# Kernel tuning notes

Hardware: AMD Instinct MI355X
Metric: run time of the kernel (lower is better)

The kernel has to match this reference:

```python
import jax, jax.numpy as jnp
import numpy as np
from math import sqrt

INPUT_SIZE = 1024
HIDDEN_SIZE = 1024
OUTPUT_SIZE = 512
BATCH = 64
SEQ = 512


def _uniform(key, shape, stdv):
    return jax.random.uniform(key, shape, jnp.float32, -stdv, stdv)


def setup_inputs() -> dict:
    key = jax.random.key(0)
    ks = jax.random.split(key, 20)
    stdv = 1.0 / sqrt(HIDDEN_SIZE)
    H, I, O = HIDDEN_SIZE, INPUT_SIZE, OUTPUT_SIZE
    inp = {
        "X": jax.random.normal(ks[0], (BATCH, SEQ, I), jnp.float32),
        "c0": jnp.zeros((H, 1), jnp.float32),
        "h0": jnp.zeros((H, 1), jnp.float32),
        "w_hi": _uniform(ks[1], (H, H), stdv), "w_xi": _uniform(ks[2], (H, I), stdv),
        "b_hi": _uniform(ks[3], (H, 1), stdv), "b_xi": _uniform(ks[4], (H, 1), stdv),
        "w_hf": _uniform(ks[5], (H, H), stdv), "w_xf": _uniform(ks[6], (H, I), stdv),
        "b_hf": _uniform(ks[7], (H, 1), stdv), "b_xf": _uniform(ks[8], (H, 1), stdv),
        "w_ho": _uniform(ks[9], (H, H), stdv), "w_xo": _uniform(ks[10], (H, I), stdv),
        "b_ho": _uniform(ks[11], (H, 1), stdv), "b_xo": _uniform(ks[12], (H, 1), stdv),
        "w_hg": _uniform(ks[13], (H, H), stdv), "w_xg": _uniform(ks[14], (H, I), stdv),
        "b_hg": _uniform(ks[15], (H, 1), stdv), "b_xg": _uniform(ks[16], (H, 1), stdv),
        "w": _uniform(ks[17], (O, H), stdv),
    }
    return inp


def reference(X, c0, h0,
              w_hi, w_xi, b_hi, b_xi,
              w_hf, w_xf, b_hf, b_xf,
              w_ho, w_xo, b_ho, b_xo,
              w_hg, w_xg, b_hg, b_xg, w):
    B = X.shape[0]
    # state kept as (B, H); biases squeezed to (H,)
    bi = (b_hi + b_xi)[:, 0]
    bf = (b_hf + b_xf)[:, 0]
    bo = (b_ho + b_xo)[:, 0]
    bg = (b_hg + b_xg)[:, 0]
    h0b = jnp.broadcast_to(h0[:, 0], (B, h0.shape[0]))
    c0b = jnp.broadcast_to(c0[:, 0], (B, c0.shape[0]))

    def step(carry, x_t):  # x_t: (B, I)
        h, c = carry
        i = jax.nn.sigmoid(h @ w_hi.T + x_t @ w_xi.T + bi)
        f = jax.nn.sigmoid(h @ w_hf.T + x_t @ w_xf.T + bf)
        o = jax.nn.sigmoid(h @ w_ho.T + x_t @ w_xo.T + bo)
        g = jnp.tanh(h @ w_hg.T + x_t @ w_xg.T + bg)
        c = f * c + i * g
        h = o * jnp.tanh(c)
        return (h, c), None

    (h, c), _ = jax.lax.scan(step, (h0b, c0b), jnp.swapaxes(X, 0, 1))
    out = h @ w.T  # (B, O)
    return out[:, :, None]  # match torch output shape (B, O, 1)
```

## Files before the change

kernel.cpp:

```cpp
#include <hip/hip_runtime.h>


typedef short short8 __attribute__((ext_vector_type(8)));
typedef float f32x4 __attribute__((ext_vector_type(4)));

typedef __attribute__((address_space(1))) const unsigned int glb_u32;
typedef __attribute__((address_space(3))) unsigned int lds_u32;

#define SEQL  512
#define POISON 0xFFFFFFFFFFFFFFFFull
#define BUFU64 16384

__device__ __forceinline__ unsigned short f2bf(float f) {
    unsigned int u = __builtin_bit_cast(unsigned int, f);
    u += 0x7FFFu + ((u >> 16) & 1u);
    return (unsigned short)(u >> 16);
}
__device__ __forceinline__ float bf2f(unsigned short s) {
    unsigned int u = ((unsigned int)s) << 16;
    return __builtin_bit_cast(float, u);
}
__device__ __forceinline__ float sigmoidf_fast(float x) {
    return 1.f / (1.f + __expf(-x));
}
__device__ __forceinline__ float tanhf_fast(float x) {
    return 1.f - 2.f / (1.f + __expf(2.f * x));
}
__device__ __forceinline__ void gld_lds16(const unsigned short* g, unsigned short* l) {
    __builtin_amdgcn_global_load_lds((glb_u32*)g, (lds_u32*)l, 16, 0, 0);
}

__global__ void k_pack_w(const float* __restrict__ w0, const float* __restrict__ w1,
                         const float* __restrict__ w2, const float* __restrict__ w3,
                         unsigned short* __restrict__ dst) {
    int idx4 = blockIdx.x * blockDim.x + threadIdx.x;
    int np = idx4 >> 8;
    int k4 = (idx4 & 255) * 4;
    int g = np & 3, r = np >> 2;
    const float* src = (g == 0) ? w0 : (g == 1) ? w1 : (g == 2) ? w2 : w3;
    float4 v = *(const float4*)(src + r * 1024 + k4);
    ushort4 o;
    o.x = f2bf(v.x); o.y = f2bf(v.y); o.z = f2bf(v.z); o.w = f2bf(v.w);
    *(ushort4*)(dst + (size_t)np * 1024 + k4) = o;
}

__global__ void k_misc(const float* __restrict__ b_hi, const float* __restrict__ b_xi,
                       const float* __restrict__ b_hf, const float* __restrict__ b_xf,
                       const float* __restrict__ b_ho, const float* __restrict__ b_xo,
                       const float* __restrict__ b_hg, const float* __restrict__ b_xg,
                       const float* __restrict__ h0, const float* __restrict__ w,
                       float* __restrict__ bias, unsigned short* __restrict__ hbuf,
                       float* __restrict__ wT) {
    int idx = blockIdx.x * blockDim.x + threadIdx.x;
    if (idx < 4096) {
        int g = idx & 3, r = idx >> 2;
        const float* bh = (g == 0) ? b_hi : (g == 1) ? b_hf : (g == 2) ? b_ho : b_hg;
        const float* bx = (g == 0) ? b_xi : (g == 1) ? b_xf : (g == 2) ? b_xo : b_xg;
        bias[idx] = bh[r] + bx[r];
    } else if (idx < 4096 + 65536) {
        int e = idx - 4096;
        int cg = e >> 8;
        int h16 = e & 15;
        hbuf[e] = f2bf(h0[(cg & 63) * 16 + h16]);
    } else if (idx < 4096 + 65536 + 524288) {
        int e = idx - 69632;
        int k = e >> 9, o = e & 511;
        wT[e] = w[o * 1024 + k];
    } else if (idx < 4096 + 65536 + 524288 + 3 * BUFU64) {
        int e = idx - (4096 + 65536 + 524288);
        ((unsigned long long*)hbuf)[BUFU64 + e] = POISON;
    }
}

__global__ void k_convert_x(const float* __restrict__ X, unsigned short* __restrict__ Xb) {
    int idx = blockIdx.x * blockDim.x + threadIdx.x;
    float4 v = ((const float4*)X)[idx];
    ushort4 o;
    o.x = f2bf(v.x); o.y = f2bf(v.y); o.z = f2bf(v.z); o.w = f2bf(v.w);
    ((ushort4*)Xb)[idx] = o;
}

__global__ __launch_bounds__(256, 1) void k_rec(const unsigned short* __restrict__ Wh,
                                                const unsigned short* __restrict__ Wx,
                                                const unsigned short* __restrict__ Xb,
                                                const float* __restrict__ bias,
                                                const float* __restrict__ c0,
                                                unsigned short* __restrict__ hbuf) {
    const int blk = blockIdx.x;
    const int jb  = blk & 3;
    const int ibb = blk >> 2;
    const int tid = threadIdx.x;
    const int w   = tid >> 6;
    const int l   = tid & 63;
    const int l15 = l & 15, lq = l >> 4;

    __shared__ unsigned short hTl[16 * 1032];
    __shared__ unsigned short xTl[16 * 1032];
    __shared__ unsigned short hTr[16 * 20];

    short8 afragH[32], afragX[32];
    {
        const unsigned short* wrH = Wh + (size_t)(ibb * 64 + w * 16 + l15) * 1024;
        const unsigned short* wrX = Wx + (size_t)(ibb * 64 + w * 16 + l15) * 1024;
#pragma unroll
        for (int ks = 0; ks < 32; ++ks)
            afragH[ks] = *(const short8*)(wrH + ks * 32 + lq * 8);
#pragma unroll
        for (int ks = 0; ks < 32; ++ks)
            afragX[ks] = *(const short8*)(wrX + ks * 32 + lq * 8);
#pragma unroll
        for (int ks = 0; ks < 32; ++ks)
            asm volatile("" : "+v"(afragH[ks]));
    }

    const int hid = ibb * 16 + w * 4 + lq;
    float c = c0[hid];
    float bias4[4];
#pragma unroll
    for (int rr = 0; rr < 4; ++rr)
        bias4[rr] = bias[(size_t)ibb * 64 + w * 16 + lq * 4 + rr];

    unsigned long long* hb64 = (unsigned long long*)hbuf;

    const int sbb = (tid >> 2) & 15, sl4 = tid & 3;
    const int stage_sh = sbb * 1032 + w * 16 + sl4 * 4;

#pragma unroll
    for (int i = 0; i < 8; ++i) {
        int r = w * 8 + i, b16 = r >> 1, half = r & 1;
        const unsigned short* src =
            Xb + ((size_t)(jb * 16 + b16) * 512 + 0) * 1024 + half * 512 + l * 8;
        gld_lds16(src, &xTl[b16 * 1032 + half * 512]);
    }
    asm volatile("s_waitcnt vmcnt(0)" ::: "memory");
    __syncthreads();

    float xg[4];
    {
        f32x4 xa0 = {0.f, 0.f, 0.f, 0.f}, xa1 = {0.f, 0.f, 0.f, 0.f};
#pragma unroll
        for (int ks = 0; ks < 32; ks += 2) {
            short8 b0 = *(const short8*)(&xTl[l15 * 1032 + ks * 32 + lq * 8]);
            short8 b1 = *(const short8*)(&xTl[l15 * 1032 + (ks + 1) * 32 + lq * 8]);
            xa0 = __builtin_amdgcn_mfma_f32_16x16x32_bf16(afragX[ks], b0, xa0, 0, 0, 0);
            xa1 = __builtin_amdgcn_mfma_f32_16x16x32_bf16(afragX[ks + 1], b1, xa1, 0, 0, 0);
        }
#pragma unroll
        for (int rr = 0; rr < 4; ++rr)
            xg[rr] = xa0[rr] + xa1[rr] + bias4[rr];
    }

    for (int t = 0; t < SEQL; ++t) {
        {
            const unsigned long long* src =
                hb64 + (size_t)(t & 3) * BUFU64 + (size_t)jb * 4096 + tid;
            unsigned long long tmp[16];
#pragma unroll
            for (int p = 0; p < 16; ++p)
                tmp[p] = __hip_atomic_load(src + p * 256, __ATOMIC_RELAXED,
                                           __HIP_MEMORY_SCOPE_AGENT);
            for (;;) {
                unsigned miss = 0;
#pragma unroll
                for (int p = 0; p < 16; ++p)
                    if (tmp[p] == POISON) miss |= 1u << p;
                if (!miss) break;
                __builtin_amdgcn_s_sleep(1);
#pragma unroll
                for (int p = 0; p < 16; ++p)
                    if (miss & (1u << p))
                        tmp[p] = __hip_atomic_load(src + p * 256, __ATOMIC_RELAXED,
                                                   __HIP_MEMORY_SCOPE_AGENT);
            }
#pragma unroll
            for (int p = 0; p < 16; ++p)
                *(unsigned long long*)(&hTl[stage_sh + p * 64]) = tmp[p];
        }
        __syncthreads();

        if (t < SEQL - 1) {
#pragma unroll
            for (int i = 0; i < 8; ++i) {
                int r = w * 8 + i, b16 = r >> 1, half = r & 1;
                const unsigned short* src =
                    Xb + ((size_t)(jb * 16 + b16) * 512 + (t + 1)) * 1024 + half * 512 + l * 8;
                gld_lds16(src, &xTl[b16 * 1032 + half * 512]);
            }
        }

        {
            f32x4 a0 = {0.f, 0.f, 0.f, 0.f}, a1 = {0.f, 0.f, 0.f, 0.f};
#pragma unroll
            for (int ks = 0; ks < 32; ks += 2) {
                short8 b0 = *(const short8*)(&hTl[l15 * 1032 + ks * 32 + lq * 8]);
                short8 b1 = *(const short8*)(&hTl[l15 * 1032 + (ks + 1) * 32 + lq * 8]);
                a0 = __builtin_amdgcn_mfma_f32_16x16x32_bf16(afragH[ks], b0, a0, 0, 0, 0);
                a1 = __builtin_amdgcn_mfma_f32_16x16x32_bf16(afragH[ks + 1], b1, a1, 0, 0, 0);
            }
            float pi = a0[0] + a1[0] + xg[0];
            float pf = a0[1] + a1[1] + xg[1];
            float po = a0[2] + a1[2] + xg[2];
            float pg = a0[3] + a1[3] + xg[3];
            float ig = sigmoidf_fast(pi);
            float fg = sigmoidf_fast(pf);
            float og = sigmoidf_fast(po);
            float gg = tanhf_fast(pg);
            c = fg * c + ig * gg;
            float hh = og * tanhf_fast(c);
            hTr[l15 * 20 + w * 4 + lq] = f2bf(hh);
        }
        __syncthreads();

        if (tid < 64) {
            int b = tid >> 2, l4 = tid & 3;
            unsigned long long v = *(const unsigned long long*)(&hTr[b * 20 + l4 * 4]);
            asm volatile("s_waitcnt vmcnt(0)" ::: "memory");
            size_t u = (size_t)(jb * 64 + ibb) * 64 + b * 4 + l4;
            __hip_atomic_store(hb64 + (size_t)((t + 1) & 3) * BUFU64 + u, v,
                               __ATOMIC_RELAXED, __HIP_MEMORY_SCOPE_AGENT);
            __hip_atomic_store(hb64 + (size_t)((t + 3) & 3) * BUFU64 + u, POISON,
                               __ATOMIC_RELAXED, __HIP_MEMORY_SCOPE_AGENT);
        }

        if (t < SEQL - 1) {
            f32x4 xa0 = {0.f, 0.f, 0.f, 0.f}, xa1 = {0.f, 0.f, 0.f, 0.f};
#pragma unroll
            for (int ks = 0; ks < 32; ks += 2) {
                short8 b0 = *(const short8*)(&xTl[l15 * 1032 + ks * 32 + lq * 8]);
                short8 b1 = *(const short8*)(&xTl[l15 * 1032 + (ks + 1) * 32 + lq * 8]);
                xa0 = __builtin_amdgcn_mfma_f32_16x16x32_bf16(afragX[ks], b0, xa0, 0, 0, 0);
                xa1 = __builtin_amdgcn_mfma_f32_16x16x32_bf16(afragX[ks + 1], b1, xa1, 0, 0, 0);
            }
#pragma unroll
            for (int rr = 0; rr < 4; ++rr)
                xg[rr] = xa0[rr] + xa1[rr] + bias4[rr];
        }
    }
}

__global__ __launch_bounds__(256) void k_out(const unsigned short* __restrict__ hT,
                                             const float* __restrict__ wT,
                                             float* __restrict__ out) {
    const int b = blockIdx.x;
    const int jb = b >> 4, b16 = b & 15;
    const int tid = threadIdx.x;
    __shared__ float hs[1024];
#pragma unroll
    for (int p = 0; p < 4; ++p) {
        int k = p * 256 + tid;
        hs[k] = bf2f(hT[(size_t)(jb * 64 + (k >> 4)) * 256 + b16 * 16 + (k & 15)]);
    }
    __syncthreads();
    float a0 = 0.f, a1 = 0.f;
    for (int k = 0; k < 1024; ++k) {
        float hv = hs[k];
        a0 = fmaf(hv, wT[k * 512 + tid], a0);
        a1 = fmaf(hv, wT[k * 512 + 256 + tid], a1);
    }
    out[b * 512 + tid] = a0;
    out[b * 512 + 256 + tid] = a1;
}

extern "C" void kernel_launch(void* const* d_in, const int* in_sizes, int n_in,
                              void* d_out, int out_size, void* d_ws, size_t ws_size,
                              hipStream_t stream) {
    const float* X    = (const float*)d_in[0];
    const float* c0   = (const float*)d_in[1];
    const float* h0   = (const float*)d_in[2];
    const float* w_hi = (const float*)d_in[3];
    const float* w_xi = (const float*)d_in[4];
    const float* b_hi = (const float*)d_in[5];
    const float* b_xi = (const float*)d_in[6];
    const float* w_hf = (const float*)d_in[7];
    const float* w_xf = (const float*)d_in[8];
    const float* b_hf = (const float*)d_in[9];
    const float* b_xf = (const float*)d_in[10];
    const float* w_ho = (const float*)d_in[11];
    const float* w_xo = (const float*)d_in[12];
    const float* b_ho = (const float*)d_in[13];
    const float* b_xo = (const float*)d_in[14];
    const float* w_hg = (const float*)d_in[15];
    const float* w_xg = (const float*)d_in[16];
    const float* b_hg = (const float*)d_in[17];
    const float* b_xg = (const float*)d_in[18];
    const float* w    = (const float*)d_in[19];

    char* ws = (char*)d_ws;
    size_t off = 0;
    unsigned short* Whp = (unsigned short*)(ws + off); off += (size_t)4096 * 1024 * 2;
    unsigned short* Wxp = (unsigned short*)(ws + off); off += (size_t)4096 * 1024 * 2;
    unsigned short* Xb  = (unsigned short*)(ws + off); off += (size_t)64 * 512 * 1024 * 2;
    float*          bias= (float*)(ws + off);          off += (size_t)4096 * 4;
    float*          wT  = (float*)(ws + off);          off += (size_t)1024 * 512 * 4;
    unsigned short* hbuf= (unsigned short*)(ws + off); off += (size_t)4 * 64 * 1024 * 2;
    if (ws_size < off) return;

    k_pack_w<<<4096, 256, 0, stream>>>(w_hi, w_hf, w_ho, w_hg, Whp);
    k_pack_w<<<4096, 256, 0, stream>>>(w_xi, w_xf, w_xo, w_xg, Wxp);
    k_misc<<<(4096 + 65536 + 524288 + 3 * BUFU64 + 255) / 256, 256, 0, stream>>>(
        b_hi, b_xi, b_hf, b_xf, b_ho, b_xo, b_hg, b_xg, h0, w, bias, hbuf, wT);
    k_convert_x<<<33554432 / 4 / 256, 256, 0, stream>>>(X, Xb);

    k_rec<<<dim3(256), dim3(256), 0, stream>>>(Whp, Wxp, Xb, bias, c0, hbuf);

    k_out<<<64, 256, 0, stream>>>(hbuf, wT, (float*)d_out);
}
```

Measured before the change: 1.820 ms.

## Split recurrent kernel into hidden and input warp groups with pipelined x-projection

Doubles the block size of the recurrent kernel so four warps hold the recurrent weight fragments and four separate warps hold the input weight fragments. The input-projection warps prefetch X two steps ahead and compute the next step's x-gates into a double-buffered LDS array while the hidden warps poll for h and run the recurrent MFMA plus gate math. This takes the x-projection off the serial critical path and halves per-thread register pressure from weight fragments. In exchange, block-wide syncs now include twice as many waves, and the pipeline adds warm-up iterations.

```diff
diff --git a/kernel.cpp b/kernel.cpp
--- a/kernel.cpp
+++ b/kernel.cpp
@@ -80,7 +80,7 @@
     ((ushort4*)Xb)[idx] = o;
 }
 
-__global__ __launch_bounds__(256, 1) void k_rec(const unsigned short* __restrict__ Wh,
+__global__ __launch_bounds__(512, 1) void k_rec(const unsigned short* __restrict__ Wh,
                                                 const unsigned short* __restrict__ Wx,
                                                 const unsigned short* __restrict__ Xb,
                                                 const float* __restrict__ bias,
@@ -91,123 +91,144 @@
     const int ibb = blk >> 2;
     const int tid = threadIdx.x;
     const int w   = tid >> 6;
+    const int wq  = w & 3;
+    const bool hw = (w < 4);
     const int l   = tid & 63;
     const int l15 = l & 15, lq = l >> 4;
 
     __shared__ unsigned short hTl[16 * 1032];
     __shared__ unsigned short xTl[16 * 1032];
+    __shared__ f32x4 xgbuf[2][256];
     __shared__ unsigned short hTr[16 * 20];
 
-    short8 afragH[32], afragX[32];
+    short8 afrag[32];
     {
-        const unsigned short* wrH = Wh + (size_t)(ibb * 64 + w * 16 + l15) * 1024;
-        const unsigned short* wrX = Wx + (size_t)(ibb * 64 + w * 16 + l15) * 1024;
+        const unsigned short* wsrc = hw ? Wh : Wx;
+        const unsigned short* wrow = wsrc + (size_t)(ibb * 64 + wq * 16 + l15) * 1024;
 #pragma unroll
         for (int ks = 0; ks < 32; ++ks)
-            afragH[ks] = *(const short8*)(wrH + ks * 32 + lq * 8);
+            afrag[ks] = *(const short8*)(wrow + ks * 32 + lq * 8);
 #pragma unroll
         for (int ks = 0; ks < 32; ++ks)
-            afragX[ks] = *(const short8*)(wrX + ks * 32 + lq * 8);
-#pragma unroll
-        for (int ks = 0; ks < 32; ++ks)
-            asm volatile("" : "+v"(afragH[ks]));
-    }
-
-    const int hid = ibb * 16 + w * 4 + lq;
+            asm volatile("" : "+v"(afrag[ks]));
+    }
+
+    const int hid = ibb * 16 + wq * 4 + lq;
     float c = c0[hid];
     float bias4[4];
 #pragma unroll
     for (int rr = 0; rr < 4; ++rr)
-        bias4[rr] = bias[(size_t)ibb * 64 + w * 16 + lq * 4 + rr];
+        bias4[rr] = bias[(size_t)ibb * 64 + wq * 16 + lq * 4 + rr];
 
     unsigned long long* hb64 = (unsigned long long*)hbuf;
 
-    const int sbb = (tid >> 2) & 15, sl4 = tid & 3;
-    const int stage_sh = sbb * 1032 + w * 16 + sl4 * 4;
-
-#pragma unroll
-    for (int i = 0; i < 8; ++i) {
-        int r = w * 8 + i, b16 = r >> 1, half = r & 1;
-        const unsigned short* src =
-            Xb + ((size_t)(jb * 16 + b16) * 512 + 0) * 1024 + half * 512 + l * 8;
-        gld_lds16(src, &xTl[b16 * 1032 + half * 512]);
-    }
-    asm volatile("s_waitcnt vmcnt(0)" ::: "memory");
-    __syncthreads();
-
-    float xg[4];
-    {
-        f32x4 xa0 = {0.f, 0.f, 0.f, 0.f}, xa1 = {0.f, 0.f, 0.f, 0.f};
-#pragma unroll
-        for (int ks = 0; ks < 32; ks += 2) {
-            short8 b0 = *(const short8*)(&xTl[l15 * 1032 + ks * 32 + lq * 8]);
-            short8 b1 = *(const short8*)(&xTl[l15 * 1032 + (ks + 1) * 32 + lq * 8]);
-            xa0 = __builtin_amdgcn_mfma_f32_16x16x32_bf16(afragX[ks], b0, xa0, 0, 0, 0);
-            xa1 = __builtin_amdgcn_mfma_f32_16x16x32_bf16(afragX[ks + 1], b1, xa1, 0, 0, 0);
-        }
-#pragma unroll
-        for (int rr = 0; rr < 4; ++rr)
-            xg[rr] = xa0[rr] + xa1[rr] + bias4[rr];
-    }
-
-    for (int t = 0; t < SEQL; ++t) {
-        {
-            const unsigned long long* src =
-                hb64 + (size_t)(t & 3) * BUFU64 + (size_t)jb * 4096 + tid;
-            unsigned long long tmp[16];
-#pragma unroll
-            for (int p = 0; p < 16; ++p)
-                tmp[p] = __hip_atomic_load(src + p * 256, __ATOMIC_RELAXED,
-                                           __HIP_MEMORY_SCOPE_AGENT);
-            for (;;) {
-                unsigned miss = 0;
+    const int stage_sh = ((tid >> 2) & 15) * 1032 + wq * 16 + (tid & 3) * 4;
+
+    for (int t = -3; t < SEQL; ++t) {
+        if (t >= 0) {
+            if (hw) {
+                const unsigned long long* src =
+                    hb64 + (size_t)(t & 3) * BUFU64 + (size_t)jb * 4096 + tid;
+                unsigned long long tmp[16];
 #pragma unroll
                 for (int p = 0; p < 16; ++p)
-                    if (tmp[p] == POISON) miss |= 1u << p;
-                if (!miss) break;
-                __builtin_amdgcn_s_sleep(1);
+                    tmp[p] = __hip_atomic_load(src + p * 256, __ATOMIC_RELAXED,
+                                               __HIP_MEMORY_SCOPE_AGENT);
+                for (;;) {
+                    unsigned miss = 0;
+#pragma unroll
+                    for (int p = 0; p < 16; ++p)
+                        if (tmp[p] == POISON) miss |= 1u << p;
+                    if (!miss) break;
+                    __builtin_amdgcn_s_sleep(1);
+#pragma unroll
+                    for (int p = 0; p < 16; ++p)
+                        if (miss & (1u << p))
+                            tmp[p] = __hip_atomic_load(src + p * 256, __ATOMIC_RELAXED,
+                                                       __HIP_MEMORY_SCOPE_AGENT);
+                }
 #pragma unroll
                 for (int p = 0; p < 16; ++p)
-                    if (miss & (1u << p))
-                        tmp[p] = __hip_atomic_load(src + p * 256, __ATOMIC_RELAXED,
-                                                   __HIP_MEMORY_SCOPE_AGENT);
-            }
-#pragma unroll
-            for (int p = 0; p < 16; ++p)
-                *(unsigned long long*)(&hTl[stage_sh + p * 64]) = tmp[p];
+                    *(unsigned long long*)(&hTl[stage_sh + p * 64]) = tmp[p];
+            } else if (t < SEQL - 1) {
+                f32x4 xa0 = {0.f, 0.f, 0.f, 0.f}, xa1 = {0.f, 0.f, 0.f, 0.f};
+#pragma unroll
+                for (int ks = 0; ks < 32; ks += 2) {
+                    short8 b0 = *(const short8*)(&xTl[l15 * 1032 + ks * 32 + lq * 8]);
+                    short8 b1 = *(const short8*)(&xTl[l15 * 1032 + (ks + 1) * 32 + lq * 8]);
+                    xa0 = __builtin_amdgcn_mfma_f32_16x16x32_bf16(afrag[ks], b0, xa0, 0, 0, 0);
+                    xa1 = __builtin_amdgcn_mfma_f32_16x16x32_bf16(afrag[ks + 1], b1, xa1, 0, 0, 0);
+                }
+                f32x4 xg4;
+#pragma unroll
+                for (int rr = 0; rr < 4; ++rr)
+                    xg4[rr] = xa0[rr] + xa1[rr] + bias4[rr];
+                xgbuf[(t + 1) & 1][wq * 64 + l] = xg4;
+            }
+        } else if (t == -3 || t == -1) {
+            if (!hw) {
+                const int tt = (t == -3) ? 0 : 1;
+#pragma unroll
+                for (int i = 0; i < 8; ++i) {
+                    int r = wq * 8 + i, b16 = r >> 1, half = r & 1;
+                    const unsigned short* src =
+                        Xb + ((size_t)(jb * 16 + b16) * 512 + tt) * 1024 + half * 512 + l * 8;
+                    gld_lds16(src, &xTl[b16 * 1032 + half * 512]);
+                }
+                asm volatile("s_waitcnt vmcnt(0)" ::: "memory");
+            }
+        } else {
+            if (!hw) {
+                f32x4 xa0 = {0.f, 0.f, 0.f, 0.f}, xa1 = {0.f, 0.f, 0.f, 0.f};
+#pragma unroll
+                for (int ks = 0; ks < 32; ks += 2) {
+                    short8 b0 = *(const short8*)(&xTl[l15 * 1032 + ks * 32 + lq * 8]);
+                    short8 b1 = *(const short8*)(&xTl[l15 * 1032 + (ks + 1) * 32 + lq * 8]);
+                    xa0 = __builtin_amdgcn_mfma_f32_16x16x32_bf16(afrag[ks], b0, xa0, 0, 0, 0);
+                    xa1 = __builtin_amdgcn_mfma_f32_16x16x32_bf16(afrag[ks + 1], b1, xa1, 0, 0, 0);
+                }
+                f32x4 xg4;
+#pragma unroll
+                for (int rr = 0; rr < 4; ++rr)
+                    xg4[rr] = xa0[rr] + xa1[rr] + bias4[rr];
+                xgbuf[0][wq * 64 + l] = xg4;
+            }
         }
         __syncthreads();
-
-        if (t < SEQL - 1) {
-#pragma unroll
-            for (int i = 0; i < 8; ++i) {
-                int r = w * 8 + i, b16 = r >> 1, half = r & 1;
-                const unsigned short* src =
-                    Xb + ((size_t)(jb * 16 + b16) * 512 + (t + 1)) * 1024 + half * 512 + l * 8;
-                gld_lds16(src, &xTl[b16 * 1032 + half * 512]);
-            }
-        }
-
-        {
+        if (t < 0) continue;
+
+        if (hw) {
+            f32x4 xg4 = xgbuf[t & 1][wq * 64 + l];
             f32x4 a0 = {0.f, 0.f, 0.f, 0.f}, a1 = {0.f, 0.f, 0.f, 0.f};
 #pragma unroll
             for (int ks = 0; ks < 32; ks += 2) {
                 short8 b0 = *(const short8*)(&hTl[l15 * 1032 + ks * 32 + lq * 8]);
                 short8 b1 = *(const short8*)(&hTl[l15 * 1032 + (ks + 1) * 32 + lq * 8]);
-                a0 = __builtin_amdgcn_mfma_f32_16x16x32_bf16(afragH[ks], b0, a0, 0, 0, 0);
-                a1 = __builtin_amdgcn_mfma_f32_16x16x32_bf16(afragH[ks + 1], b1, a1, 0, 0, 0);
-            }
-            float pi = a0[0] + a1[0] + xg[0];
-            float pf = a0[1] + a1[1] + xg[1];
-            float po = a0[2] + a1[2] + xg[2];
-            float pg = a0[3] + a1[3] + xg[3];
+                a0 = __builtin_amdgcn_mfma_f32_16x16x32_bf16(afrag[ks], b0, a0, 0, 0, 0);
+                a1 = __builtin_amdgcn_mfma_f32_16x16x32_bf16(afrag[ks + 1], b1, a1, 0, 0, 0);
+            }
+            float pi = a0[0] + a1[0] + xg4[0];
+            float pf = a0[1] + a1[1] + xg4[1];
+            float po = a0[2] + a1[2] + xg4[2];
+            float pg = a0[3] + a1[3] + xg4[3];
             float ig = sigmoidf_fast(pi);
             float fg = sigmoidf_fast(pf);
             float og = sigmoidf_fast(po);
             float gg = tanhf_fast(pg);
             c = fg * c + ig * gg;
             float hh = og * tanhf_fast(c);
-            hTr[l15 * 20 + w * 4 + lq] = f2bf(hh);
+            hTr[l15 * 20 + wq * 4 + lq] = f2bf(hh);
+        } else {
+            if (t < SEQL - 2) {
+#pragma unroll
+                for (int i = 0; i < 8; ++i) {
+                    int r = wq * 8 + i, b16 = r >> 1, half = r & 1;
+                    const unsigned short* src =
+                        Xb + ((size_t)(jb * 16 + b16) * 512 + (t + 2)) * 1024 + half * 512 + l * 8;
+                    gld_lds16(src, &xTl[b16 * 1032 + half * 512]);
+                }
+            }
+            asm volatile("s_waitcnt vmcnt(0)" ::: "memory");
         }
         __syncthreads();
 
@@ -220,20 +241,6 @@
                                __ATOMIC_RELAXED, __HIP_MEMORY_SCOPE_AGENT);
             __hip_atomic_store(hb64 + (size_t)((t + 3) & 3) * BUFU64 + u, POISON,
                                __ATOMIC_RELAXED, __HIP_MEMORY_SCOPE_AGENT);
-        }
-
-        if (t < SEQL - 1) {
-            f32x4 xa0 = {0.f, 0.f, 0.f, 0.f}, xa1 = {0.f, 0.f, 0.f, 0.f};
-#pragma unroll
-            for (int ks = 0; ks < 32; ks += 2) {
-                short8 b0 = *(const short8*)(&xTl[l15 * 1032 + ks * 32 + lq * 8]);
-                short8 b1 = *(const short8*)(&xTl[l15 * 1032 + (ks + 1) * 32 + lq * 8]);
-                xa0 = __builtin_amdgcn_mfma_f32_16x16x32_bf16(afragX[ks], b0, xa0, 0, 0, 0);
-                xa1 = __builtin_amdgcn_mfma_f32_16x16x32_bf16(afragX[ks + 1], b1, xa1, 0, 0, 0);
-            }
-#pragma unroll
-            for (int rr = 0; rr < 4; ++rr)
-                xg[rr] = xa0[rr] + xa1[rr] + bias4[rr];
         }
     }
 }
@@ -301,7 +308,7 @@
         b_hi, b_xi, b_hf, b_xf, b_ho, b_xo, b_hg, b_xg, h0, w, bias, hbuf, wT);
     k_convert_x<<<33554432 / 4 / 256, 256, 0, stream>>>(X, Xb);
 
-    k_rec<<<dim3(256), dim3(256), 0, stream>>>(Whp, Wxp, Xb, bias, c0, hbuf);
+    k_rec<<<dim3(256), dim3(512), 0, stream>>>(Whp, Wxp, Xb, bias, c0, hbuf);
 
     k_out<<<64, 256, 0, stream>>>(hbuf, wT, (float*)d_out);
 }
```

New measurement: 1.938 ms. 1.06x slower.
